# Kernel tuning notes

Measured on AMD Instinct MI355X. Metric: run time of the kernel, lower is better.

## Reference

```python
import jax, jax.numpy as jnp
import numpy as np

# ----- static layer configuration (mirrors __init__ / _precompute_cg_tensor) -----
NODE_LS = [0, 0, 1, 1]          # node_l_values (multiplicity expressed via repetition; node_multiplicity=1)
EDGE_SH = 1                      # edge_sh_degree
H_LS = NODE_LS + NODE_LS + [0]   # l-values of h = [f_src, f_tgt, d]
H_DIMS = [2 * l + 1 for l in H_LS]
H_OFF = np.concatenate([[0], np.cumsum(H_DIMS)])
A_DIMS = [2 * l + 1 for l in range(EDGE_SH + 1)]
A_OFF = np.concatenate([[0], np.cumsum(A_DIMS)])
O_DIMS = [2 * l + 1 for l in NODE_LS]
O_OFF = np.concatenate([[0], np.cumsum(O_DIMS)])
F_DIM = int(O_OFF[-1])           # 8
A_DIM = int(A_OFF[-1])           # 4
N_NODES, N_EDGES = 100000, 1600000
MLP_DIMS = [2 * len(NODE_LS) + 1, 64, 32, len(NODE_LS)]  # 9 -> 64 -> 32 -> 4

def _levi_civita():
    e = np.zeros((3, 3, 3), np.float32)
    e[0, 1, 2] = e[1, 2, 0] = e[2, 0, 1] = 1.0
    e[0, 2, 1] = e[2, 1, 0] = e[1, 0, 2] = -1.0
    return e

# real SO(3) Clebsch-Gordan tensors (e3nn wigner_3j normalization: full contraction norm 1)
_CG = {
    (0, 0, 0): np.ones((1, 1, 1), np.float32),
    (0, 1, 1): (np.eye(3, dtype=np.float32) / np.sqrt(3.0)).reshape(1, 3, 3),
    (1, 0, 1): (np.eye(3, dtype=np.float32) / np.sqrt(3.0)).reshape(3, 1, 3),
    (1, 1, 0): (np.eye(3, dtype=np.float32) / np.sqrt(3.0)).reshape(3, 3, 1),
    (1, 1, 1): _levi_civita() / np.sqrt(6.0),
}

CONNECTIONS = []  # (h_idx, a_l, out_idx, cg[h,a,o]) -- same enumeration order as the torch loop
for _h_idx, _hl in enumerate(H_LS):
    for _al in range(EDGE_SH + 1):
        for _oi, _ol in enumerate(NODE_LS):
            if abs(_hl - _al) <= _ol <= _hl + _al and (_hl, _al, _ol) in _CG:
                CONNECTIONS.append((_h_idx, _al, _oi, jnp.asarray(_CG[(_hl, _al, _ol)])))


def _invariants(x):
    # s_i = [f_{l=0}, ||f_{l=1}||, ...] per l-slot (multiplicity 1)
    outs = []
    for i, l in enumerate(NODE_LS):
        s, e = int(O_OFF[i]), int(O_OFF[i + 1])
        if l == 0:
            outs.append(x[:, s:e])
        else:
            outs.append(jnp.linalg.norm(x[:, s:e], axis=1, keepdims=True))
    return jnp.concatenate(outs, axis=1)


def setup_inputs() -> dict:
    ks = jax.random.split(jax.random.key(0), 10)
    edge_index = jax.random.randint(ks[0], (2, N_EDGES), 0, N_NODES)
    f = jax.random.normal(ks[1], (N_NODES, F_DIM), jnp.float32)
    d = jax.random.uniform(ks[2], (N_EDGES, 1), jnp.float32)
    a = jax.random.normal(ks[3], (N_EDGES, A_DIM), jnp.float32)
    w1 = jax.random.normal(ks[4], (EDGE_SH + 1,), jnp.float32) * 0.1
    w2 = jax.random.normal(ks[5], (EDGE_SH + 1,), jnp.float32) * 0.1
    W0 = jax.random.normal(ks[6], (MLP_DIMS[0], MLP_DIMS[1]), jnp.float32) / np.sqrt(MLP_DIMS[0])
    b0 = jnp.zeros((MLP_DIMS[1],), jnp.float32)
    W1 = jax.random.normal(ks[7], (MLP_DIMS[1], MLP_DIMS[2]), jnp.float32) / np.sqrt(MLP_DIMS[1])
    b1 = jnp.zeros((MLP_DIMS[2],), jnp.float32)
    W2 = jax.random.normal(ks[8], (MLP_DIMS[2], MLP_DIMS[3]), jnp.float32) / np.sqrt(MLP_DIMS[2])
    b2 = jnp.zeros((MLP_DIMS[3],), jnp.float32)
    return {"edge_index": edge_index, "f": f, "d": d, "a": a, "w1": w1, "w2": w2,
            "W0": W0, "b0": b0, "W1": W1, "b1": b1, "W2": W2, "b2": b2}


def reference(edge_index, f, d, a, w1, w2, W0, b0, W1, b1, W2, b2):
    src, tgt = edge_index[0], edge_index[1]
    n = f.shape[0]
    h = jnp.concatenate([f[src], f[tgt], d], axis=1)  # [E, 17]
    messages = jnp.zeros((h.shape[0], F_DIM), f.dtype)
    for h_idx, a_l, out_idx, cg in CONNECTIONS:
        hs, he = int(H_OFF[h_idx]), int(H_OFF[h_idx + 1])
        as_, ae = int(A_OFF[a_l]), int(A_OFF[a_l + 1])
        os_, oe = int(O_OFF[out_idx]), int(O_OFF[out_idx + 1])
        raw = jnp.einsum('hao,eh,ea->eo', cg, h[:, hs:he], a[:, as_:ae])  # [E, 2*out_l+1]
        msg = jnp.tanh(w2[a_l] * jnp.tanh(w1[a_l] * raw))
        messages = messages.at[:, os_:oe].add(msg)
    agg = jax.ops.segment_sum(messages, tgt, num_segments=n)          # [N, 8]
    dist_sum = jax.ops.segment_sum(d, tgt, num_segments=n)           # [N, 1]
    counts = jax.ops.segment_sum(jnp.ones((h.shape[0],), f.dtype), tgt, num_segments=n)
    avg_d = dist_sum / (counts[:, None] + 1e-8)
    psi_in = jnp.concatenate([_invariants(f), _invariants(agg), avg_d], axis=1)  # [N, 9]
    x = jax.nn.relu(psi_in @ W0 + b0)
    x = jax.nn.relu(x @ W1 + b1)
    gates = jax.nn.sigmoid(x @ W2 + b2)  # [N, 4]
    gate_full = jnp.concatenate(
        [jnp.repeat(gates[:, i:i + 1], O_DIMS[i], axis=1) for i in range(len(NODE_LS))], axis=1)
    return f + gate_full * agg
```

## Files before the change

### kernel.cpp

```cpp
#include <hip/hip_runtime.h>
#include <math.h>

#define IS3 0.57735026918962576f
#define IS6 0.40824829046386302f

#define SHIFT 11
#define BSZ   2048
#define CAP   36864u
#define SEG   6
#define MQ    4096.0f
#define IMQ   (1.0f/4096.0f)

__device__ __forceinline__ float fastrcp(float x) { return __builtin_amdgcn_rcpf(x); }

__device__ __forceinline__ float ftanh(float x) {
    float e = __expf(2.0f * x);
    return 1.0f - 2.0f * fastrcp(e + 1.0f);
}

__device__ __forceinline__ float Tnl(float x, float w1, float w2) {
    return ftanh(w2 * ftanh(w1 * x));
}

__device__ __forceinline__ int q16(float x) {
    int v = (int)rintf(x * MQ);
    v = v >  32767 ?  32767 : v;
    v = v < -32768 ? -32768 : v;
    return v;
}

__global__ __launch_bounds__(1024) void route_kernel(
    const int* __restrict__ ei, const float* __restrict__ f,
    const float* __restrict__ d, const float* __restrict__ a,
    const float* __restrict__ w1p, const float* __restrict__ w2p,
    unsigned* __restrict__ tails,
    unsigned* __restrict__ qmeta,
    uint2* __restrict__ qmsg,
    int E, int nbuk)
{
    __shared__ unsigned hcnt[64];
    __shared__ unsigned hoff[64];
    int tid = threadIdx.x;
    if (tid < 64) hcnt[tid] = 0;
    __syncthreads();

    int e = blockIdx.x * 1024 + tid;
    bool valid = (e < E);
    int t = 0;
    unsigned b = 0, lrank = 0;
    if (valid) {
        t = ei[E + e];
        b = ((unsigned)t) >> SHIFT;
        lrank = atomicAdd(&hcnt[b], 1u);
    }
    __syncthreads();

    unsigned basek = 0;
    if (tid < nbuk && hcnt[tid] != 0u)
        basek = atomicAdd(&tails[tid * 64], hcnt[tid]);

    unsigned dq = 0;
    uint2 pk = make_uint2(0u, 0u);
    if (valid) {
        int s = ei[e];
        float w10 = w1p[0], w11 = w1p[1], w20 = w2p[0], w21 = w2p[1];

        const float4* f4 = (const float4*)f;
        float4 sA = f4[2*s], sB = f4[2*s+1];
        float4 tA = f4[2*t], tB = f4[2*t+1];
        float de = d[e];
        float4 av = ((const float4*)a)[e];
        float a0 = av.x, ax = av.y, ay = av.z, az = av.w;

        float sc[5] = { sA.x, sA.y, tA.x, tA.y, de };
        float vx[4] = { sA.z, sB.y, tA.z, tB.y };
        float vy[4] = { sA.w, sB.z, tA.w, tB.z };
        float vz[4] = { sB.x, sB.w, tB.x, tB.w };

        float mS = 0.f, mX = 0.f, mY = 0.f, mZ = 0.f;
        #pragma unroll
        for (int i = 0; i < 5; ++i) {
            mS += Tnl(sc[i] * a0, w10, w20);
            mX += Tnl(sc[i] * ax * IS3, w11, w21);
            mY += Tnl(sc[i] * ay * IS3, w11, w21);
            mZ += Tnl(sc[i] * az * IS3, w11, w21);
        }
        #pragma unroll
        for (int i = 0; i < 4; ++i) {
            float dva = vx[i]*ax + vy[i]*ay + vz[i]*az;
            mS += Tnl(dva * IS3, w11, w21);
            mX += Tnl(vx[i] * a0 * IS3, w10, w20);
            mY += Tnl(vy[i] * a0 * IS3, w10, w20);
            mZ += Tnl(vz[i] * a0 * IS3, w10, w20);
            float cx = vy[i]*az - vz[i]*ay;
            float cy = vz[i]*ax - vx[i]*az;
            float cz = vx[i]*ay - vy[i]*ax;
            mX += Tnl(cx * IS6, w11, w21);
            mY += Tnl(cy * IS6, w11, w21);
            mZ += Tnl(cz * IS6, w11, w21);
        }

        unsigned dqi = (unsigned)(de * 2047.0f + 0.5f);
        dq = dqi > 2047u ? 2047u : dqi;
        int qS = q16(mS), qX = q16(mX), qY = q16(mY), qZ = q16(mZ);
        pk.x = ((unsigned)(unsigned short)qS) | (((unsigned)(unsigned short)qX) << 16);
        pk.y = ((unsigned)(unsigned short)qY) | (((unsigned)(unsigned short)qZ) << 16);
    }

    if (tid < nbuk) hoff[tid] = basek;
    __syncthreads();

    if (valid) {
        unsigned pos = hoff[b] + lrank;
        if (pos < CAP) {
            size_t idx = (size_t)b * CAP + pos;
            qmeta[idx] = (((unsigned)(t & (BSZ - 1))) << 11) | dq;
            qmsg[idx]  = pk;
        }
    }
}

__global__ __launch_bounds__(1024) void bucket_kernel(
    const unsigned* __restrict__ tails, const unsigned* __restrict__ qmeta,
    const uint2* __restrict__ qmsg, float* __restrict__ partial, int nbuk)
{
    __shared__ int acc[BSZ * 6];
    int wg = blockIdx.x;
    int b = wg / SEG, sgi = wg % SEG;
    for (int i = threadIdx.x; i < BSZ * 6; i += 1024) acc[i] = 0;
    __syncthreads();

    unsigned tail = tails[b * 64];
    if (tail > CAP) tail = CAP;
    unsigned lo = (unsigned)(((unsigned long long)tail * sgi) / SEG);
    unsigned hi = (unsigned)(((unsigned long long)tail * (sgi + 1)) / SEG);
    size_t base = (size_t)b * CAP;

    for (unsigned q = lo + threadIdx.x; q < hi; q += 1024) {
        unsigned meta = qmeta[base + q];
        uint2 m = qmsg[base + q];
        int local = (int)(meta >> 11);
        int* p = &acc[local * 6];
        atomicAdd(p + 0, (int)(short)(m.x & 0xFFFFu));
        atomicAdd(p + 1, (int)(short)(m.x >> 16));
        atomicAdd(p + 2, (int)(short)(m.y & 0xFFFFu));
        atomicAdd(p + 3, (int)(short)(m.y >> 16));
        atomicAdd(p + 4, (int)((1u << 20) | (meta & 2047u)));
    }
    __syncthreads();

    float* dst = partial + (size_t)wg * (BSZ * 6);
    for (int i = threadIdx.x; i < BSZ * 6; i += 1024) {
        int k = i % 6;
        int v = acc[i];
        dst[i] = (k < 4) ? (float)v * IMQ : __int_as_float(v);
    }
}

__global__ __launch_bounds__(256) void mlp_kernel(
    const float* __restrict__ f, const float* __restrict__ partial,
    const float* __restrict__ W0, const float* __restrict__ b0,
    const float* __restrict__ W1, const float* __restrict__ b1,
    const float* __restrict__ W2, const float* __restrict__ b2,
    float* __restrict__ out, int N)
{
    __shared__ float sW0[9*64];
    __shared__ float sb0[64];
    __shared__ float sW1[64*32];
    __shared__ float sb1[32];
    __shared__ float sW2[32*4];
    __shared__ float sb2[4];
    for (int i = threadIdx.x; i < 9*64;  i += 256) sW0[i] = W0[i];
    for (int i = threadIdx.x; i < 64;    i += 256) sb0[i] = b0[i];
    for (int i = threadIdx.x; i < 64*32; i += 256) sW1[i] = W1[i];
    for (int i = threadIdx.x; i < 32;    i += 256) sb1[i] = b1[i];
    for (int i = threadIdx.x; i < 32*4;  i += 256) sW2[i] = W2[i];
    for (int i = threadIdx.x; i < 4;     i += 256) sb2[i] = b2[i];
    __syncthreads();

    int n = blockIdx.x * 256 + threadIdx.x;
    if (n >= N) return;

    int b = n >> SHIFT;
    int local = n & (BSZ - 1);
    float aS = 0.f, ax = 0.f, ay = 0.f, az = 0.f;
    int packed = 0;
    #pragma unroll
    for (int s2 = 0; s2 < SEG; ++s2) {
        const float* p = partial + ((size_t)(b * SEG + s2)) * (BSZ * 6)
                       + (size_t)local * 6;
        aS += p[0]; ax += p[1]; ay += p[2]; az += p[3];
        packed += __float_as_int(p[4]);
    }
    float cf = (float)(packed >> 20);
    float dsum = (float)(packed & 0xFFFFF) * (1.0f / 2047.0f);

    float4 fA = ((const float4*)f)[2*n];
    float4 fB = ((const float4*)f)[2*n+1];

    float psi[9];
    psi[0] = fA.x; psi[1] = fA.y;
    psi[2] = sqrtf(fA.z*fA.z + fA.w*fA.w + fB.x*fB.x);
    psi[3] = sqrtf(fB.y*fB.y + fB.z*fB.z + fB.w*fB.w);
    psi[4] = aS; psi[5] = aS;
    float nv = sqrtf(ax*ax + ay*ay + az*az);
    psi[6] = nv; psi[7] = nv;
    psi[8] = dsum * fastrcp(cf + 1e-8f);

    float x1[32];
    #pragma unroll
    for (int j = 0; j < 32; ++j) x1[j] = sb1[j];
    #pragma unroll
    for (int i = 0; i < 64; ++i) {
        float acc = sb0[i];
        #pragma unroll
        for (int k = 0; k < 9; ++k) acc += psi[k] * sW0[k*64 + i];
        acc = fmaxf(acc, 0.f);
        #pragma unroll
        for (int j = 0; j < 32; ++j) x1[j] += acc * sW1[i*32 + j];
    }
    #pragma unroll
    for (int j = 0; j < 32; ++j) x1[j] = fmaxf(x1[j], 0.f);

    float g[4];
    #pragma unroll
    for (int j = 0; j < 4; ++j) {
        float acc = sb2[j];
        #pragma unroll
        for (int i = 0; i < 32; ++i) acc += x1[i] * sW2[i*4 + j];
        g[j] = fastrcp(1.0f + __expf(-acc));
    }

    float* o = out + (size_t)8*n;
    o[0] = fA.x + g[0]*aS;
    o[1] = fA.y + g[1]*aS;
    o[2] = fA.z + g[2]*ax;
    o[3] = fA.w + g[2]*ay;
    o[4] = fB.x + g[2]*az;
    o[5] = fB.y + g[3]*ax;
    o[6] = fB.z + g[3]*ay;
    o[7] = fB.w + g[3]*az;
}

extern "C" void kernel_launch(void* const* d_in, const int* in_sizes, int n_in,
                              void* d_out, int out_size, void* d_ws, size_t ws_size,
                              hipStream_t stream) {
    const int*   ei = (const int*)d_in[0];
    const float* f  = (const float*)d_in[1];
    const float* d  = (const float*)d_in[2];
    const float* a  = (const float*)d_in[3];
    const float* w1 = (const float*)d_in[4];
    const float* w2 = (const float*)d_in[5];
    const float* W0 = (const float*)d_in[6];
    const float* b0 = (const float*)d_in[7];
    const float* W1 = (const float*)d_in[8];
    const float* b1 = (const float*)d_in[9];
    const float* W2 = (const float*)d_in[10];
    const float* b2 = (const float*)d_in[11];
    int E = in_sizes[0] / 2;
    int N = in_sizes[1] / 8;
    int nbuk = (N + BSZ - 1) >> SHIFT;

    char* w = (char*)d_ws;
    size_t qn = (size_t)nbuk * CAP;
    uint2*    qmsg    = (uint2*)w;
    unsigned* qmeta   = (unsigned*)(w + qn * 8);
    float*    partial = (float*)(w + qn * 12);
    unsigned* tails   = (unsigned*)(w + qn * 12
                        + (size_t)nbuk * SEG * BSZ * 6 * 4);

    hipMemsetAsync(tails, 0, (size_t)nbuk * 64 * sizeof(unsigned), stream);

    int EB = (E + 1023) / 1024;
    route_kernel <<<dim3(EB), dim3(1024), 0, stream>>>(
        ei, f, d, a, w1, w2, tails, qmeta, qmsg, E, nbuk);
    bucket_kernel<<<dim3(nbuk * SEG), dim3(1024), 0, stream>>>(
        tails, qmeta, qmsg, partial, nbuk);
    mlp_kernel   <<<dim3((N + 255) / 256), dim3(256), 0, stream>>>(
        f, partial, W0, b0, W1, b1, W2, b2, (float*)d_out, N);
}
```

Baseline: 182.5 us.

## Approximate outer tanh with polynomial, pack bucket atomics into 64-bit, drop MLP LDS staging

The outer tanh of the per-edge nonlinearity becomes a cubic/quintic Taylor polynomial, and the factor of 2 is folded into w1 ahead of time. This removes one exp and one reciprocal per term, but it is only accurate while w2*tanh(...) stays small. The bucket kernel now packs two 32-bit counters, biased to keep the low halves non-negative, into one 64-bit LDS atomic, cutting five atomics per edge to three. Partial sums are written as integers in a structure-of-arrays layout, and the MLP undoes the bias. The MLP kernel no longer stages weights in shared memory and reads them straight from global or constant cache.

Result: slower. 205.1 us (+12.4%).

```diff
diff --git a/kernel.cpp b/kernel.cpp
--- a/kernel.cpp
+++ b/kernel.cpp
@@ -13,13 +13,13 @@
 
 __device__ __forceinline__ float fastrcp(float x) { return __builtin_amdgcn_rcpf(x); }
 
-__device__ __forceinline__ float ftanh(float x) {
-    float e = __expf(2.0f * x);
-    return 1.0f - 2.0f * fastrcp(e + 1.0f);
-}
-
-__device__ __forceinline__ float Tnl(float x, float w1, float w2) {
-    return ftanh(w2 * ftanh(w1 * x));
+__device__ __forceinline__ float Tnl(float x, float tw1, float w2) {
+    float e = __expf(tw1 * x);
+    float u = 1.0f - 2.0f * fastrcp(e + 1.0f);
+    float z = w2 * u;
+    float z2 = z * z;
+    float p = __builtin_fmaf(z2, 0.133333333f, -0.333333333f);
+    return __builtin_fmaf(z * z2, p, z);
 }
 
 __device__ __forceinline__ int q16(float x) {
@@ -63,7 +63,8 @@
     uint2 pk = make_uint2(0u, 0u);
     if (valid) {
         int s = ei[e];
-        float w10 = w1p[0], w11 = w1p[1], w20 = w2p[0], w21 = w2p[1];
+        float tw10 = 2.0f * w1p[0], tw11 = 2.0f * w1p[1];
+        float w20 = w2p[0], w21 = w2p[1];
 
         const float4* f4 = (const float4*)f;
         float4 sA = f4[2*s], sB = f4[2*s+1];
@@ -80,24 +81,24 @@
         float mS = 0.f, mX = 0.f, mY = 0.f, mZ = 0.f;
         #pragma unroll
         for (int i = 0; i < 5; ++i) {
-            mS += Tnl(sc[i] * a0, w10, w20);
-            mX += Tnl(sc[i] * ax * IS3, w11, w21);
-            mY += Tnl(sc[i] * ay * IS3, w11, w21);
-            mZ += Tnl(sc[i] * az * IS3, w11, w21);
+            mS += Tnl(sc[i] * a0, tw10, w20);
+            mX += Tnl(sc[i] * ax * IS3, tw11, w21);
+            mY += Tnl(sc[i] * ay * IS3, tw11, w21);
+            mZ += Tnl(sc[i] * az * IS3, tw11, w21);
         }
         #pragma unroll
         for (int i = 0; i < 4; ++i) {
             float dva = vx[i]*ax + vy[i]*ay + vz[i]*az;
-            mS += Tnl(dva * IS3, w11, w21);
-            mX += Tnl(vx[i] * a0 * IS3, w10, w20);
-            mY += Tnl(vy[i] * a0 * IS3, w10, w20);
-            mZ += Tnl(vz[i] * a0 * IS3, w10, w20);
+            mS += Tnl(dva * IS3, tw11, w21);
+            mX += Tnl(vx[i] * a0 * IS3, tw10, w20);
+            mY += Tnl(vy[i] * a0 * IS3, tw10, w20);
+            mZ += Tnl(vz[i] * a0 * IS3, tw10, w20);
             float cx = vy[i]*az - vz[i]*ay;
             float cy = vz[i]*ax - vx[i]*az;
             float cz = vx[i]*ay - vy[i]*ax;
-            mX += Tnl(cx * IS6, w11, w21);
-            mY += Tnl(cy * IS6, w11, w21);
-            mZ += Tnl(cz * IS6, w11, w21);
+            mX += Tnl(cx * IS6, tw11, w21);
+            mY += Tnl(cy * IS6, tw11, w21);
+            mZ += Tnl(cz * IS6, tw11, w21);
         }
 
         unsigned dqi = (unsigned)(de * 2047.0f + 0.5f);
@@ -122,12 +123,16 @@
 
 __global__ __launch_bounds__(1024) void bucket_kernel(
     const unsigned* __restrict__ tails, const unsigned* __restrict__ qmeta,
-    const uint2* __restrict__ qmsg, float* __restrict__ partial, int nbuk)
+    const uint2* __restrict__ qmsg, unsigned* __restrict__ partial, int nbuk)
 {
-    __shared__ int acc[BSZ * 6];
+    __shared__ unsigned long long accSX[BSZ];
+    __shared__ unsigned long long accYZ[BSZ];
+    __shared__ unsigned accM[BSZ];
     int wg = blockIdx.x;
     int b = wg / SEG, sgi = wg % SEG;
-    for (int i = threadIdx.x; i < BSZ * 6; i += 1024) acc[i] = 0;
+    for (int i = threadIdx.x; i < BSZ; i += 1024) {
+        accSX[i] = 0ull; accYZ[i] = 0ull; accM[i] = 0u;
+    }
     __syncthreads();
 
     unsigned tail = tails[b * 64];
@@ -140,60 +145,60 @@
         unsigned meta = qmeta[base + q];
         uint2 m = qmsg[base + q];
         int local = (int)(meta >> 11);
-        int* p = &acc[local * 6];
-        atomicAdd(p + 0, (int)(short)(m.x & 0xFFFFu));
-        atomicAdd(p + 1, (int)(short)(m.x >> 16));
-        atomicAdd(p + 2, (int)(short)(m.y & 0xFFFFu));
-        atomicAdd(p + 3, (int)(short)(m.y >> 16));
-        atomicAdd(p + 4, (int)((1u << 20) | (meta & 2047u)));
-    }
-    __syncthreads();
-
-    float* dst = partial + (size_t)wg * (BSZ * 6);
-    for (int i = threadIdx.x; i < BSZ * 6; i += 1024) {
-        int k = i % 6;
-        int v = acc[i];
-        dst[i] = (k < 4) ? (float)v * IMQ : __int_as_float(v);
+        int qS = (int)(short)(m.x & 0xFFFFu);
+        int qX = (int)(short)(m.x >> 16);
+        int qY = (int)(short)(m.y & 0xFFFFu);
+        int qZ = (int)(short)(m.y >> 16);
+        unsigned long long vSX =
+            (((unsigned long long)(unsigned)qX) << 32) | (unsigned)(qS + 65536);
+        unsigned long long vYZ =
+            (((unsigned long long)(unsigned)qZ) << 32) | (unsigned)(qY + 65536);
+        atomicAdd(&accSX[local], vSX);
+        atomicAdd(&accYZ[local], vYZ);
+        atomicAdd(&accM[local], (1u << 20) | (meta & 2047u));
+    }
+    __syncthreads();
+
+    unsigned* dst = partial + (size_t)wg * (BSZ * 5);
+    for (int i = threadIdx.x; i < BSZ; i += 1024) {
+        unsigned long long sx = accSX[i], yz = accYZ[i];
+        dst[0*BSZ + i] = (unsigned)sx;
+        dst[1*BSZ + i] = (unsigned)(sx >> 32);
+        dst[2*BSZ + i] = (unsigned)yz;
+        dst[3*BSZ + i] = (unsigned)(yz >> 32);
+        dst[4*BSZ + i] = accM[i];
     }
 }
 
 __global__ __launch_bounds__(256) void mlp_kernel(
-    const float* __restrict__ f, const float* __restrict__ partial,
+    const float* __restrict__ f, const unsigned* __restrict__ partial,
     const float* __restrict__ W0, const float* __restrict__ b0,
     const float* __restrict__ W1, const float* __restrict__ b1,
     const float* __restrict__ W2, const float* __restrict__ b2,
     float* __restrict__ out, int N)
 {
-    __shared__ float sW0[9*64];
-    __shared__ float sb0[64];
-    __shared__ float sW1[64*32];
-    __shared__ float sb1[32];
-    __shared__ float sW2[32*4];
-    __shared__ float sb2[4];
-    for (int i = threadIdx.x; i < 9*64;  i += 256) sW0[i] = W0[i];
-    for (int i = threadIdx.x; i < 64;    i += 256) sb0[i] = b0[i];
-    for (int i = threadIdx.x; i < 64*32; i += 256) sW1[i] = W1[i];
-    for (int i = threadIdx.x; i < 32;    i += 256) sb1[i] = b1[i];
-    for (int i = threadIdx.x; i < 32*4;  i += 256) sW2[i] = W2[i];
-    for (int i = threadIdx.x; i < 4;     i += 256) sb2[i] = b2[i];
-    __syncthreads();
-
     int n = blockIdx.x * 256 + threadIdx.x;
     if (n >= N) return;
 
     int b = n >> SHIFT;
     int local = n & (BSZ - 1);
-    float aS = 0.f, ax = 0.f, ay = 0.f, az = 0.f;
-    int packed = 0;
+    int S = 0, X = 0, Y = 0, Z = 0, cnt = 0, dqs = 0;
     #pragma unroll
     for (int s2 = 0; s2 < SEG; ++s2) {
-        const float* p = partial + ((size_t)(b * SEG + s2)) * (BSZ * 6)
-                       + (size_t)local * 6;
-        aS += p[0]; ax += p[1]; ay += p[2]; az += p[3];
-        packed += __float_as_int(p[4]);
-    }
-    float cf = (float)(packed >> 20);
-    float dsum = (float)(packed & 0xFFFFF) * (1.0f / 2047.0f);
+        const unsigned* p = partial + ((size_t)(b * SEG + s2)) * (BSZ * 5);
+        unsigned m4 = p[4*BSZ + local];
+        int c = (int)(m4 >> 20);
+        S += (int)p[0*BSZ + local] - (c << 16);
+        X += (int)p[1*BSZ + local];
+        Y += (int)p[2*BSZ + local] - (c << 16);
+        Z += (int)p[3*BSZ + local];
+        dqs += (int)(m4 & 0xFFFFFu);
+        cnt += c;
+    }
+    float aS = (float)S * IMQ, ax = (float)X * IMQ;
+    float ay = (float)Y * IMQ, az = (float)Z * IMQ;
+    float cf = (float)cnt;
+    float dsum = (float)dqs * (1.0f / 2047.0f);
 
     float4 fA = ((const float4*)f)[2*n];
     float4 fB = ((const float4*)f)[2*n+1];
@@ -209,15 +214,15 @@
 
     float x1[32];
     #pragma unroll
-    for (int j = 0; j < 32; ++j) x1[j] = sb1[j];
+    for (int j = 0; j < 32; ++j) x1[j] = b1[j];
     #pragma unroll
     for (int i = 0; i < 64; ++i) {
-        float acc = sb0[i];
-        #pragma unroll
-        for (int k = 0; k < 9; ++k) acc += psi[k] * sW0[k*64 + i];
+        float acc = b0[i];
+        #pragma unroll
+        for (int k = 0; k < 9; ++k) acc += psi[k] * W0[k*64 + i];
         acc = fmaxf(acc, 0.f);
         #pragma unroll
-        for (int j = 0; j < 32; ++j) x1[j] += acc * sW1[i*32 + j];
+        for (int j = 0; j < 32; ++j) x1[j] += acc * W1[i*32 + j];
     }
     #pragma unroll
     for (int j = 0; j < 32; ++j) x1[j] = fmaxf(x1[j], 0.f);
@@ -225,9 +230,9 @@
     float g[4];
     #pragma unroll
     for (int j = 0; j < 4; ++j) {
-        float acc = sb2[j];
-        #pragma unroll
-        for (int i = 0; i < 32; ++i) acc += x1[i] * sW2[i*4 + j];
+        float acc = b2[j];
+        #pragma unroll
+        for (int i = 0; i < 32; ++i) acc += x1[i] * W2[i*4 + j];
         g[j] = fastrcp(1.0f + __expf(-acc));
     }
 
@@ -265,9 +270,9 @@
     size_t qn = (size_t)nbuk * CAP;
     uint2*    qmsg    = (uint2*)w;
     unsigned* qmeta   = (unsigned*)(w + qn * 8);
-    float*    partial = (float*)(w + qn * 12);
+    unsigned* partial = (unsigned*)(w + qn * 12);
     unsigned* tails   = (unsigned*)(w + qn * 12
-                        + (size_t)nbuk * SEG * BSZ * 6 * 4);
+                        + (size_t)nbuk * SEG * BSZ * 5 * 4);
 
     hipMemsetAsync(tails, 0, (size_t)nbuk * 64 * sizeof(unsigned), stream);
 
```
